# Performance work log

Measured on AMD Instinct MI355X. Metric: run time of the kernel, lower is better.

Reference implementation:

```python
import jax, jax.numpy as jnp
import numpy as np

N_NODES = 100000


def gcn_conv(x, W, b, src, dst, n_nodes):
    """PyG-style GCNConv: h = D^{-1/2} (A + I) D^{-1/2} (x @ W) + b.

    src/dst already include self-loops. Symmetric normalization with
    degrees computed on the destination index (in-degree incl. self-loop).
    """
    h = x @ W  # [N, out] - transform before propagate (cheap gather dim)
    deg = jax.ops.segment_sum(jnp.ones_like(dst, dtype=h.dtype), dst,
                              num_segments=n_nodes)  # [N]
    dinv = jnp.where(deg > 0, jax.lax.rsqrt(deg), 0.0)  # deg^{-1/2}, 0 for isolated
    norm = dinv[src] * dinv[dst]  # [E]
    msg = h[src] * norm[:, None]  # gather + normalize, [E, out]
    out = jax.ops.segment_sum(msg, dst, num_segments=n_nodes)  # scatter-sum
    return out + b


def setup_inputs() -> dict:
    key = jax.random.key(0)
    k1, k2, k3, k4 = jax.random.split(key, 4)
    in_dim, hidden, n_edges = 128, 32, 3200000
    x = jax.random.normal(k1, (N_NODES, in_dim), dtype=jnp.float32)
    edge_index = jax.random.randint(k2, (2, n_edges), 0, N_NODES, dtype=jnp.int64)
    W1 = jax.random.normal(k3, (in_dim, hidden), dtype=jnp.float32) / np.sqrt(in_dim)
    b1 = jnp.zeros((hidden,), dtype=jnp.float32)
    W2 = jax.random.normal(k4, (hidden, 1), dtype=jnp.float32) / np.sqrt(hidden)
    b2 = jnp.zeros((1,), dtype=jnp.float32)
    return {"x": x, "edge_index": edge_index, "W1": W1, "b1": b1,
            "W2": W2, "b2": b2}


def reference(x, edge_index, W1, b1, W2, b2):
    n = x.shape[0]
    loops = jnp.arange(n, dtype=edge_index.dtype)
    src = jnp.concatenate([edge_index[0], loops])  # add self-loops
    dst = jnp.concatenate([edge_index[1], loops])
    h = jax.nn.relu(gcn_conv(x, W1, b1, src, dst, n))
    out = jax.nn.sigmoid(gcn_conv(h, W2, b2, src, dst, n))
    return out.squeeze(-1)  # [N]
```

## Files before the change

kernel.cpp:

```cpp
#include <hip/hip_runtime.h>
#include <hip/hip_bf16.h>
#include <stdint.h>

#define IN_DIM 128
#define HID 32
#define CSHIFT 7
#define CNODES 128
#define NPART 8
#define SUBCAP 672
#define TILE 2048
#define EPT 8
#define NBC_MAX 800

#define FPS1 524288.0f
#define IFPS1 (1.0f / 524288.0f)
#define FPS2 262144.0f
#define IFPS2 (1.0f / 262144.0f)

__device__ __forceinline__ float bf_lo(uint u) {
    uint t = u << 16; return *(float*)&t;
}
__device__ __forceinline__ float bf_hi(uint u) {
    uint t = u & 0xFFFF0000u; return *(float*)&t;
}

__global__ __launch_bounds__(256) void binB_kernel(const int* __restrict__ src,
                                                   const int* __restrict__ dst,
                                                   int* __restrict__ pcursor,
                                                   int* __restrict__ pbuf,
                                                   int e, int nbc) {
    __shared__ int hist[NBC_MAX];
    __shared__ int gbase[NBC_MAX];
    int part = blockIdx.x & (NPART - 1);
    int base = blockIdx.x * TILE;
    int cnt = min(TILE, e - base);
    if (cnt <= 0) return;
    int tid = threadIdx.x;
    for (int i = tid; i < nbc; i += 256) hist[i] = 0;
    int s[EPT], d[EPT];
#pragma unroll
    for (int j = 0; j < EPT; j++) {
        int i = tid + 256 * j;
        bool m = i < cnt;
        d[j] = m ? dst[base + i] : -1;
        s[j] = m ? src[base + i] : 0;
    }
    __syncthreads();
#pragma unroll
    for (int j = 0; j < EPT; j++)
        if (d[j] >= 0) atomicAdd(&hist[d[j] >> CSHIFT], 1);
    __syncthreads();
    for (int i = tid; i < nbc; i += 256) {
        int c = hist[i];
        gbase[i] = (c > 0) ? atomicAdd(&pcursor[part * nbc + i], c) : 0;
        hist[i] = 0;
    }
    __syncthreads();
#pragma unroll
    for (int j = 0; j < EPT; j++) {
        if (d[j] < 0) continue;
        int bin = d[j] >> CSHIFT;
        int slot = atomicAdd(&hist[bin], 1);
        int pos = gbase[bin] + slot;
        if (pos < SUBCAP)
            pbuf[(size_t)(part * nbc + bin) * SUBCAP + pos] = s[j] | ((d[j] & (CNODES - 1)) << 17);
    }
}

__global__ __launch_bounds__(256) void deg_kernel(const int* __restrict__ pcursor,
                                                  const int* __restrict__ pbuf,
                                                  float* __restrict__ dinv_g,
                                                  int n, int nbc) {
    int b = blockIdx.x;
    __shared__ int hist[CNODES];
    int tid = threadIdx.x;
    int w = tid >> 6, lane = tid & 63;
    if (tid < CNODES) hist[tid] = 0;
    __syncthreads();
#pragma unroll
    for (int pp = 0; pp < 2; pp++) {
        int p = w + pp * 4;
        int cnt = min(pcursor[p * nbc + b], SUBCAP);
        const int* seg = pbuf + (size_t)(p * nbc + b) * SUBCAP;
        for (int i = lane; i < cnt; i += 64)
            atomicAdd(&hist[__builtin_nontemporal_load(seg + i) >> 17], 1);
    }
    __syncthreads();
    if (tid < CNODES) {
        int node = b * CNODES + tid;
        if (node < n) dinv_g[node] = rsqrtf((float)hist[tid] + 1.0f);
    }
}

__global__ __launch_bounds__(256) void mm1_kernel(const float* __restrict__ dinv,
                                                  const float* __restrict__ x,
                                                  const float* __restrict__ W1,
                                                  __hip_bfloat16* __restrict__ h1s,
                                                  int n) {
    int b = blockIdx.x;
    __shared__ float Ws[IN_DIM * 36];
    __shared__ float xs[CNODES * 36];
    int tid = threadIdx.x;
    for (int i = tid; i < IN_DIM * HID; i += 256)
        Ws[(i >> 5) * 36 + (i & 31)] = W1[i];
    int gj = tid & 7;
    int gn = tid >> 3;
    float acc[4][4];
#pragma unroll
    for (int i = 0; i < 4; i++)
#pragma unroll
        for (int j = 0; j < 4; j++) acc[i][j] = 0.f;
#pragma unroll 1
    for (int kc = 0; kc < 4; kc++) {
        __syncthreads();
#pragma unroll
        for (int t = 0; t < 4; t++) {
            int f4id = tid + 256 * t;
            int row = f4id >> 3, c4 = f4id & 7;
            int node = b * CNODES + row;
            float4 xv = make_float4(0.f, 0.f, 0.f, 0.f);
            if (node < n)
                xv = *(const float4*)(x + (size_t)node * IN_DIM + kc * 32 + c4 * 4);
            *(float4*)(xs + row * 36 + c4 * 4) = xv;
        }
        __syncthreads();
#pragma unroll
        for (int k4 = 0; k4 < 8; k4++) {
            int kb = kc * 32 + k4 * 4;
            float4 wf0 = *(const float4*)(Ws + (kb + 0) * 36 + gj * 4);
            float4 wf1 = *(const float4*)(Ws + (kb + 1) * 36 + gj * 4);
            float4 wf2 = *(const float4*)(Ws + (kb + 2) * 36 + gj * 4);
            float4 wf3 = *(const float4*)(Ws + (kb + 3) * 36 + gj * 4);
#pragma unroll
            for (int i = 0; i < 4; i++) {
                float4 xv = *(const float4*)(xs + (gn + 32 * i) * 36 + k4 * 4);
                acc[i][0] += xv.x * wf0.x + xv.y * wf1.x + xv.z * wf2.x + xv.w * wf3.x;
                acc[i][1] += xv.x * wf0.y + xv.y * wf1.y + xv.z * wf2.y + xv.w * wf3.y;
                acc[i][2] += xv.x * wf0.z + xv.y * wf1.z + xv.z * wf2.z + xv.w * wf3.z;
                acc[i][3] += xv.x * wf0.w + xv.y * wf1.w + xv.z * wf2.w + xv.w * wf3.w;
            }
        }
    }
#pragma unroll
    for (int i = 0; i < 4; i++) {
        int node = b * CNODES + gn + 32 * i;
        if (node < n) {
            float dv = dinv[node];
            __hip_bfloat162 p0 = __float22bfloat162_rn(
                make_float2(acc[i][0] * dv, acc[i][1] * dv));
            __hip_bfloat162 p1 = __float22bfloat162_rn(
                make_float2(acc[i][2] * dv, acc[i][3] * dv));
            uint2 u;
            u.x = *(uint*)&p0;
            u.y = *(uint*)&p1;
            *(uint2*)(h1s + (size_t)node * HID + gj * 4) = u;
        }
    }
}

__global__ __launch_bounds__(512) void agg1_kernel(const int* __restrict__ pcursor,
                                                   const int* __restrict__ pbuf,
                                                   const float* __restrict__ dinv,
                                                   const __hip_bfloat16* __restrict__ h1s,
                                                   const float* __restrict__ b1,
                                                   const float* __restrict__ W2,
                                                   float* __restrict__ h2s, int n, int nbc) {
    int b = blockIdx.x;
    __shared__ int acc[CNODES * 33];
    __shared__ int ls[NPART * SUBCAP];
    int tid = threadIdx.x;
    const uint* h1u = (const uint*)h1s;
    {
        int row = tid >> 4, u = tid & 15;
        for (int rr = row; rr < CNODES; rr += 32) {
            int node = b * CNODES + rr;
            uint uv = (node < n) ? h1u[(size_t)node * 16 + u] : 0u;
            acc[rr * 33 + 2 * u]     = __float2int_rn(bf_lo(uv) * FPS1);
            acc[rr * 33 + 2 * u + 1] = __float2int_rn(bf_hi(uv) * FPS1);
        }
    }
    int w = tid >> 6;
    int lane = tid & 63;
    int cnt = min(pcursor[w * nbc + b], SUBCAP);
    const int* seg = pbuf + (size_t)(w * nbc + b) * SUBCAP;
    int* lw = ls + w * SUBCAP;
    for (int i = lane; i < cnt; i += 64)
        lw[i] = __builtin_nontemporal_load(seg + i);
    __syncthreads();
    int g = lane >> 4, j2 = lane & 15;
    int nmain = cnt & ~15;
    for (int i0 = 0; i0 < nmain; i0 += 16) {
        int4 v = *(const int4*)(lw + i0 + 4 * g);
        uint uA = h1u[(size_t)(v.x & 0x1FFFF) * 16 + j2];
        uint uB = h1u[(size_t)(v.y & 0x1FFFF) * 16 + j2];
        uint uC = h1u[(size_t)(v.z & 0x1FFFF) * 16 + j2];
        uint uD = h1u[(size_t)(v.w & 0x1FFFF) * 16 + j2];
        atomicAdd(&acc[(v.x >> 17) * 33 + 2 * j2],     __float2int_rn(bf_lo(uA) * FPS1));
        atomicAdd(&acc[(v.x >> 17) * 33 + 2 * j2 + 1], __float2int_rn(bf_hi(uA) * FPS1));
        atomicAdd(&acc[(v.y >> 17) * 33 + 2 * j2],     __float2int_rn(bf_lo(uB) * FPS1));
        atomicAdd(&acc[(v.y >> 17) * 33 + 2 * j2 + 1], __float2int_rn(bf_hi(uB) * FPS1));
        atomicAdd(&acc[(v.z >> 17) * 33 + 2 * j2],     __float2int_rn(bf_lo(uC) * FPS1));
        atomicAdd(&acc[(v.z >> 17) * 33 + 2 * j2 + 1], __float2int_rn(bf_hi(uC) * FPS1));
        atomicAdd(&acc[(v.w >> 17) * 33 + 2 * j2],     __float2int_rn(bf_lo(uD) * FPS1));
        atomicAdd(&acc[(v.w >> 17) * 33 + 2 * j2 + 1], __float2int_rn(bf_hi(uD) * FPS1));
    }
    for (int i = nmain + g; i < cnt; i += 4) {
        int v = lw[i];
        uint uu = h1u[(size_t)(v & 0x1FFFF) * 16 + j2];
        atomicAdd(&acc[(v >> 17) * 33 + 2 * j2],     __float2int_rn(bf_lo(uu) * FPS1));
        atomicAdd(&acc[(v >> 17) * 33 + 2 * j2 + 1], __float2int_rn(bf_hi(uu) * FPS1));
    }
    __syncthreads();
    int node_l = tid >> 2, jp = tid & 3;
    int node = b * CNODES + node_l;
    if (node < n) {
        float dd = dinv[node];
        float pv = 0.f;
#pragma unroll
        for (int q = 0; q < 8; q++) {
            int j = jp * 8 + q;
            float v = (float)acc[node_l * 33 + j] * IFPS1 * dd + b1[j];
            v = fmaxf(v, 0.f);
            pv += v * W2[j];
        }
        pv += __shfl_xor(pv, 1);
        pv += __shfl_xor(pv, 2);
        if (jp == 0) h2s[node] = pv * dd;
    }
}

__global__ __launch_bounds__(512) void agg2_kernel(const int* __restrict__ pcursor,
                                                   const int* __restrict__ pbuf,
                                                   const float* __restrict__ dinv,
                                                   const float* __restrict__ h2s,
                                                   const float* __restrict__ b2,
                                                   float* __restrict__ out, int n, int nbc) {
    int b = blockIdx.x;
    __shared__ int acc2[CNODES];
    int tid = threadIdx.x;
    if (tid < CNODES) acc2[tid] = 0;
    __syncthreads();
    int w = tid >> 6;
    int lane = tid & 63;
    int cnt = min(pcursor[w * nbc + b], SUBCAP);
    const int* seg = pbuf + (size_t)(w * nbc + b) * SUBCAP;
    for (int i = lane; i < cnt; i += 64) {
        int v = seg[i];
        atomicAdd(&acc2[v >> 17], __float2int_rn(h2s[v & 0x1FFFF] * FPS2));
    }
    __syncthreads();
    if (tid < CNODES) {
        int node = b * CNODES + tid;
        if (node < n) {
            float val = ((float)acc2[tid] * IFPS2 + h2s[node]) * dinv[node] + b2[0];
            out[node] = 1.f / (1.f + expf(-val));
        }
    }
}

extern "C" void kernel_launch(void* const* d_in, const int* in_sizes, int n_in,
                              void* d_out, int out_size, void* d_ws, size_t ws_size,
                              hipStream_t stream) {
    const float* x  = (const float*)d_in[0];
    const int*   ei = (const int*)d_in[1];
    const float* W1 = (const float*)d_in[2];
    const float* b1 = (const float*)d_in[3];
    const float* W2 = (const float*)d_in[4];
    const float* b2 = (const float*)d_in[5];
    float* out = (float*)d_out;

    const int n = in_sizes[0] / IN_DIM;
    const int e = in_sizes[1] / 2;
    const int* src = ei;
    const int* dst = ei + e;
    const int nbc = (n + CNODES - 1) >> CSHIFT;

    int* pbuf = (int*)d_ws;
    __hip_bfloat16* h1s = (__hip_bfloat16*)(pbuf + (size_t)NPART * nbc * SUBCAP);
    float* dinv    = (float*)(h1s + (size_t)n * HID);
    float* h2s     = dinv + n;
    int*   pcursor = (int*)(h2s + n);

    const int B = 256;
    int gBin = (e + TILE - 1) / TILE;
    int m  = NPART * nbc;

    hipMemsetAsync(pcursor, 0, (size_t)m * sizeof(int), stream);
    binB_kernel<<<gBin, B, 0, stream>>>(src, dst, pcursor, pbuf, e, nbc);
    deg_kernel<<<nbc, B, 0, stream>>>(pcursor, pbuf, dinv, n, nbc);
    mm1_kernel<<<nbc, B, 0, stream>>>(dinv, x, W1, h1s, n);
    agg1_kernel<<<nbc, 512, 0, stream>>>(pcursor, pbuf, dinv, h1s, b1, W2, h2s, n, nbc);
    agg2_kernel<<<nbc, 512, 0, stream>>>(pcursor, pbuf, dinv, h2s, b2, out, n, nbc);
}
```

Before: 238.3 us.

## Double-buffer x tiles via direct global-to-LDS loads and remap agg1 lanes

In mm1, x tiles are now loaded straight into LDS with global_load_lds, double-buffered so the next K chunk loads while the current one is computed, and stored with an XOR-swizzled layout in place of the padded one. Out-of-range rows are clamped to the last node rather than zeroed. In agg1, each lane now handles a single feature column (32 lanes per edge, two edges per wave-step), so every lane issues one LDS atomic per edge instead of two. The cost is duplicate 4-byte gathers of the same packed bf16 word by neighbouring lanes.

```diff
diff --git a/kernel.cpp b/kernel.cpp
--- a/kernel.cpp
+++ b/kernel.cpp
@@ -16,6 +16,9 @@
 #define IFPS1 (1.0f / 524288.0f)
 #define FPS2 262144.0f
 #define IFPS2 (1.0f / 262144.0f)
+
+typedef __attribute__((address_space(1))) const uint32_t gas_u32;
+typedef __attribute__((address_space(3))) uint32_t las_u32;
 
 __device__ __forceinline__ float bf_lo(uint u) {
     uint t = u << 16; return *(float*)&t;
@@ -99,10 +102,21 @@
                                                   int n) {
     int b = blockIdx.x;
     __shared__ float Ws[IN_DIM * 36];
-    __shared__ float xs[CNODES * 36];
-    int tid = threadIdx.x;
+    __shared__ float xs[2][CNODES * 32];
+    int tid = threadIdx.x;
+    int w = tid >> 6, lane = tid & 63;
     for (int i = tid; i < IN_DIM * HID; i += 256)
         Ws[(i >> 5) * 36 + (i & 31)] = W1[i];
+    int srow = (lane >> 3);
+    int scol = (lane & 7) ^ srow;
+#pragma unroll
+    for (int q = 0; q < 4; q++) {
+        int row = q * 32 + w * 8 + srow;
+        int node = min(b * CNODES + row, n - 1);
+        __builtin_amdgcn_global_load_lds(
+            (gas_u32*)(x + (size_t)node * IN_DIM + scol * 4),
+            (las_u32*)(&xs[0][(q * 32 + w * 8) * 32]), 16, 0, 0);
+    }
     int gj = tid & 7;
     int gn = tid >> 3;
     float acc[4][4];
@@ -110,20 +124,21 @@
     for (int i = 0; i < 4; i++)
 #pragma unroll
         for (int j = 0; j < 4; j++) acc[i][j] = 0.f;
+    __syncthreads();
 #pragma unroll 1
     for (int kc = 0; kc < 4; kc++) {
-        __syncthreads();
-#pragma unroll
-        for (int t = 0; t < 4; t++) {
-            int f4id = tid + 256 * t;
-            int row = f4id >> 3, c4 = f4id & 7;
-            int node = b * CNODES + row;
-            float4 xv = make_float4(0.f, 0.f, 0.f, 0.f);
-            if (node < n)
-                xv = *(const float4*)(x + (size_t)node * IN_DIM + kc * 32 + c4 * 4);
-            *(float4*)(xs + row * 36 + c4 * 4) = xv;
-        }
-        __syncthreads();
+        int cur = kc & 1;
+        if (kc < 3) {
+#pragma unroll
+            for (int q = 0; q < 4; q++) {
+                int row = q * 32 + w * 8 + srow;
+                int node = min(b * CNODES + row, n - 1);
+                __builtin_amdgcn_global_load_lds(
+                    (gas_u32*)(x + (size_t)node * IN_DIM + (kc + 1) * 32 + scol * 4),
+                    (las_u32*)(&xs[cur ^ 1][(q * 32 + w * 8) * 32]), 16, 0, 0);
+            }
+        }
+        const float* xc = xs[cur];
 #pragma unroll
         for (int k4 = 0; k4 < 8; k4++) {
             int kb = kc * 32 + k4 * 4;
@@ -131,15 +146,17 @@
             float4 wf1 = *(const float4*)(Ws + (kb + 1) * 36 + gj * 4);
             float4 wf2 = *(const float4*)(Ws + (kb + 2) * 36 + gj * 4);
             float4 wf3 = *(const float4*)(Ws + (kb + 3) * 36 + gj * 4);
+            int slot = (k4 ^ (gn & 7)) * 4;
 #pragma unroll
             for (int i = 0; i < 4; i++) {
-                float4 xv = *(const float4*)(xs + (gn + 32 * i) * 36 + k4 * 4);
+                float4 xv = *(const float4*)(xc + (gn + 32 * i) * 32 + slot);
                 acc[i][0] += xv.x * wf0.x + xv.y * wf1.x + xv.z * wf2.x + xv.w * wf3.x;
                 acc[i][1] += xv.x * wf0.y + xv.y * wf1.y + xv.z * wf2.y + xv.w * wf3.y;
                 acc[i][2] += xv.x * wf0.z + xv.y * wf1.z + xv.z * wf2.z + xv.w * wf3.z;
                 acc[i][3] += xv.x * wf0.w + xv.y * wf1.w + xv.z * wf2.w + xv.w * wf3.w;
             }
         }
+        __syncthreads();
     }
 #pragma unroll
     for (int i = 0; i < 4; i++) {
@@ -187,28 +204,33 @@
     for (int i = lane; i < cnt; i += 64)
         lw[i] = __builtin_nontemporal_load(seg + i);
     __syncthreads();
-    int g = lane >> 4, j2 = lane & 15;
-    int nmain = cnt & ~15;
-    for (int i0 = 0; i0 < nmain; i0 += 16) {
+    int g = lane >> 5;
+    int j = lane & 31;
+    int jh = j >> 1, jsel = j & 1;
+    int nmain = cnt & ~7;
+    for (int i0 = 0; i0 < nmain; i0 += 8) {
         int4 v = *(const int4*)(lw + i0 + 4 * g);
-        uint uA = h1u[(size_t)(v.x & 0x1FFFF) * 16 + j2];
-        uint uB = h1u[(size_t)(v.y & 0x1FFFF) * 16 + j2];
-        uint uC = h1u[(size_t)(v.z & 0x1FFFF) * 16 + j2];
-        uint uD = h1u[(size_t)(v.w & 0x1FFFF) * 16 + j2];
-        atomicAdd(&acc[(v.x >> 17) * 33 + 2 * j2],     __float2int_rn(bf_lo(uA) * FPS1));
-        atomicAdd(&acc[(v.x >> 17) * 33 + 2 * j2 + 1], __float2int_rn(bf_hi(uA) * FPS1));
-        atomicAdd(&acc[(v.y >> 17) * 33 + 2 * j2],     __float2int_rn(bf_lo(uB) * FPS1));
-        atomicAdd(&acc[(v.y >> 17) * 33 + 2 * j2 + 1], __float2int_rn(bf_hi(uB) * FPS1));
-        atomicAdd(&acc[(v.z >> 17) * 33 + 2 * j2],     __float2int_rn(bf_lo(uC) * FPS1));
-        atomicAdd(&acc[(v.z >> 17) * 33 + 2 * j2 + 1], __float2int_rn(bf_hi(uC) * FPS1));
-        atomicAdd(&acc[(v.w >> 17) * 33 + 2 * j2],     __float2int_rn(bf_lo(uD) * FPS1));
-        atomicAdd(&acc[(v.w >> 17) * 33 + 2 * j2 + 1], __float2int_rn(bf_hi(uD) * FPS1));
-    }
-    for (int i = nmain + g; i < cnt; i += 4) {
-        int v = lw[i];
-        uint uu = h1u[(size_t)(v & 0x1FFFF) * 16 + j2];
-        atomicAdd(&acc[(v >> 17) * 33 + 2 * j2],     __float2int_rn(bf_lo(uu) * FPS1));
-        atomicAdd(&acc[(v >> 17) * 33 + 2 * j2 + 1], __float2int_rn(bf_hi(uu) * FPS1));
+        uint uA = h1u[(size_t)(v.x & 0x1FFFF) * 16 + jh];
+        uint uB = h1u[(size_t)(v.y & 0x1FFFF) * 16 + jh];
+        uint uC = h1u[(size_t)(v.z & 0x1FFFF) * 16 + jh];
+        uint uD = h1u[(size_t)(v.w & 0x1FFFF) * 16 + jh];
+        float fA = jsel ? bf_hi(uA) : bf_lo(uA);
+        float fB = jsel ? bf_hi(uB) : bf_lo(uB);
+        float fC = jsel ? bf_hi(uC) : bf_lo(uC);
+        float fD = jsel ? bf_hi(uD) : bf_lo(uD);
+        atomicAdd(&acc[(v.x >> 17) * 33 + j], __float2int_rn(fA * FPS1));
+        atomicAdd(&acc[(v.y >> 17) * 33 + j], __float2int_rn(fB * FPS1));
+        atomicAdd(&acc[(v.z >> 17) * 33 + j], __float2int_rn(fC * FPS1));
+        atomicAdd(&acc[(v.w >> 17) * 33 + j], __float2int_rn(fD * FPS1));
+    }
+    for (int i = nmain; i < cnt; i += 2) {
+        int idx = i + g;
+        if (idx < cnt) {
+            int v = lw[idx];
+            uint u = h1u[(size_t)(v & 0x1FFFF) * 16 + jh];
+            float f = jsel ? bf_hi(u) : bf_lo(u);
+            atomicAdd(&acc[(v >> 17) * 33 + j], __float2int_rn(f * FPS1));
+        }
     }
     __syncthreads();
     int node_l = tid >> 2, jp = tid & 3;
@@ -218,10 +240,10 @@
         float pv = 0.f;
 #pragma unroll
         for (int q = 0; q < 8; q++) {
-            int j = jp * 8 + q;
-            float v = (float)acc[node_l * 33 + j] * IFPS1 * dd + b1[j];
+            int jj = jp * 8 + q;
+            float v = (float)acc[node_l * 33 + jj] * IFPS1 * dd + b1[jj];
             v = fmaxf(v, 0.f);
-            pv += v * W2[j];
+            pv += v * W2[jj];
         }
         pv += __shfl_xor(pv, 1);
         pv += __shfl_xor(pv, 2);
```

After: 246.3 us. 1.03x slower.

## Double-buffer x tiles via global_load_lds and vectorize agg2 edge loads

Applied to the files above, without the earlier changes.

The mm1 kernel now streams x tiles straight into LDS with the async global_load_lds builtin. It double-buffers the K chunks so the next chunk loads while the current one is multiplied, and uses an XOR-swizzled 32-float row layout in place of the padded 36-float layout to avoid bank conflicts. The agg2 kernel reads four packed edges per int4 load and issues the four gathers before their atomics, which adds memory-level parallelism. Out-of-range rows are clamped to n-1 rather than zeroed; this stays correct only because those rows are never written back.

```diff
diff --git a/kernel.cpp b/kernel.cpp
--- a/kernel.cpp
+++ b/kernel.cpp
@@ -16,6 +16,9 @@
 #define IFPS1 (1.0f / 524288.0f)
 #define FPS2 262144.0f
 #define IFPS2 (1.0f / 262144.0f)
+
+typedef __attribute__((address_space(1))) const uint32_t gas_u32;
+typedef __attribute__((address_space(3))) uint32_t las_u32;
 
 __device__ __forceinline__ float bf_lo(uint u) {
     uint t = u << 16; return *(float*)&t;
@@ -99,10 +102,21 @@
                                                   int n) {
     int b = blockIdx.x;
     __shared__ float Ws[IN_DIM * 36];
-    __shared__ float xs[CNODES * 36];
-    int tid = threadIdx.x;
+    __shared__ float xs[2][CNODES * 32];
+    int tid = threadIdx.x;
+    int w = tid >> 6, lane = tid & 63;
     for (int i = tid; i < IN_DIM * HID; i += 256)
         Ws[(i >> 5) * 36 + (i & 31)] = W1[i];
+    int srow = (lane >> 3);
+    int scol = (lane & 7) ^ srow;
+#pragma unroll
+    for (int q = 0; q < 4; q++) {
+        int row = q * 32 + w * 8 + srow;
+        int node = min(b * CNODES + row, n - 1);
+        __builtin_amdgcn_global_load_lds(
+            (gas_u32*)(x + (size_t)node * IN_DIM + scol * 4),
+            (las_u32*)(&xs[0][(q * 32 + w * 8) * 32]), 16, 0, 0);
+    }
     int gj = tid & 7;
     int gn = tid >> 3;
     float acc[4][4];
@@ -110,20 +124,21 @@
     for (int i = 0; i < 4; i++)
 #pragma unroll
         for (int j = 0; j < 4; j++) acc[i][j] = 0.f;
+    __syncthreads();
 #pragma unroll 1
     for (int kc = 0; kc < 4; kc++) {
-        __syncthreads();
-#pragma unroll
-        for (int t = 0; t < 4; t++) {
-            int f4id = tid + 256 * t;
-            int row = f4id >> 3, c4 = f4id & 7;
-            int node = b * CNODES + row;
-            float4 xv = make_float4(0.f, 0.f, 0.f, 0.f);
-            if (node < n)
-                xv = *(const float4*)(x + (size_t)node * IN_DIM + kc * 32 + c4 * 4);
-            *(float4*)(xs + row * 36 + c4 * 4) = xv;
-        }
-        __syncthreads();
+        int cur = kc & 1;
+        if (kc < 3) {
+#pragma unroll
+            for (int q = 0; q < 4; q++) {
+                int row = q * 32 + w * 8 + srow;
+                int node = min(b * CNODES + row, n - 1);
+                __builtin_amdgcn_global_load_lds(
+                    (gas_u32*)(x + (size_t)node * IN_DIM + (kc + 1) * 32 + scol * 4),
+                    (las_u32*)(&xs[cur ^ 1][(q * 32 + w * 8) * 32]), 16, 0, 0);
+            }
+        }
+        const float* xc = xs[cur];
 #pragma unroll
         for (int k4 = 0; k4 < 8; k4++) {
             int kb = kc * 32 + k4 * 4;
@@ -131,15 +146,17 @@
             float4 wf1 = *(const float4*)(Ws + (kb + 1) * 36 + gj * 4);
             float4 wf2 = *(const float4*)(Ws + (kb + 2) * 36 + gj * 4);
             float4 wf3 = *(const float4*)(Ws + (kb + 3) * 36 + gj * 4);
+            int slot = (k4 ^ (gn & 7)) * 4;
 #pragma unroll
             for (int i = 0; i < 4; i++) {
-                float4 xv = *(const float4*)(xs + (gn + 32 * i) * 36 + k4 * 4);
+                float4 xv = *(const float4*)(xc + (gn + 32 * i) * 32 + slot);
                 acc[i][0] += xv.x * wf0.x + xv.y * wf1.x + xv.z * wf2.x + xv.w * wf3.x;
                 acc[i][1] += xv.x * wf0.y + xv.y * wf1.y + xv.z * wf2.y + xv.w * wf3.y;
                 acc[i][2] += xv.x * wf0.z + xv.y * wf1.z + xv.z * wf2.z + xv.w * wf3.z;
                 acc[i][3] += xv.x * wf0.w + xv.y * wf1.w + xv.z * wf2.w + xv.w * wf3.w;
             }
         }
+        __syncthreads();
     }
 #pragma unroll
     for (int i = 0; i < 4; i++) {
@@ -244,8 +261,21 @@
     int lane = tid & 63;
     int cnt = min(pcursor[w * nbc + b], SUBCAP);
     const int* seg = pbuf + (size_t)(w * nbc + b) * SUBCAP;
-    for (int i = lane; i < cnt; i += 64) {
-        int v = seg[i];
+    int nq = cnt >> 2;
+    for (int q = lane; q < nq; q += 64) {
+        int4 v = *(const int4*)(seg + 4 * q);
+        float f0 = h2s[v.x & 0x1FFFF];
+        float f1 = h2s[v.y & 0x1FFFF];
+        float f2 = h2s[v.z & 0x1FFFF];
+        float f3 = h2s[v.w & 0x1FFFF];
+        atomicAdd(&acc2[v.x >> 17], __float2int_rn(f0 * FPS2));
+        atomicAdd(&acc2[v.y >> 17], __float2int_rn(f1 * FPS2));
+        atomicAdd(&acc2[v.z >> 17], __float2int_rn(f2 * FPS2));
+        atomicAdd(&acc2[v.w >> 17], __float2int_rn(f3 * FPS2));
+    }
+    int rem = cnt & 3;
+    if (lane < rem) {
+        int v = seg[4 * nq + lane];
         atomicAdd(&acc2[v >> 17], __float2int_rn(h2s[v & 0x1FFFF] * FPS2));
     }
     __syncthreads();
```

New measurement: 222.7 us. 6.5% less time.
